# Performance work log

Measured on AMD Instinct MI355X. Metric: run time of the kernel, lower is better.

## Reference

```python
import jax, jax.numpy as jnp
import numpy as np

N_NODES = 40000
N_EDGES = 640000
NODE_D = 128
EDGE_D = 64
OUT_D = 128


def setup_inputs() -> dict:
    key = jax.random.key(0)
    ks = jax.random.split(key, 8)
    return {
        "node_features": jax.random.normal(ks[0], (N_NODES, NODE_D), dtype=jnp.float32),
        "edge_features": jax.random.normal(ks[1], (N_EDGES, EDGE_D), dtype=jnp.float32),
        "src": jax.random.randint(ks[2], (N_EDGES,), 0, N_NODES, dtype=jnp.int32),
        "dst": jax.random.randint(ks[3], (N_EDGES,), 0, N_NODES, dtype=jnp.int32),
        "W_msg_w": jax.random.normal(ks[4], (OUT_D, NODE_D + EDGE_D), dtype=jnp.float32) * 0.05,
        "W_msg_b": jax.random.normal(ks[5], (OUT_D,), dtype=jnp.float32) * 0.05,
        "W_apply_w": jax.random.normal(ks[6], (OUT_D, OUT_D + NODE_D), dtype=jnp.float32) * 0.05,
        "W_apply_b": jax.random.normal(ks[7], (OUT_D,), dtype=jnp.float32) * 0.05,
    }


def reference(node_features, edge_features, src, dst, W_msg_w, W_msg_b, W_apply_w, W_apply_b):
    n_nodes = node_features.shape[0]
    # message: gather src node feats, concat edge feats, linear + relu  [E, OUT_D]
    msg_in = jnp.concatenate([node_features[src], edge_features], axis=-1)
    m = jax.nn.relu(msg_in @ W_msg_w.T + W_msg_b)
    # aggregate: sum messages into destination nodes  [N, OUT_D]
    h_neigh = jax.ops.segment_sum(m, dst, num_segments=n_nodes)
    # apply: concat original node feats with aggregated messages, linear + relu
    apply_in = jnp.concatenate([node_features, h_neigh], axis=-1)
    return jax.nn.relu(apply_in @ W_apply_w.T + W_apply_b)
```

## Files before the change

kernel.cpp:

```cpp
#include <hip/hip_runtime.h>
#include <stdint.h>

#define NN 40000
#define NE 640000
#define ND 128
#define ED 64
#define OD 128
#define KM 192
#define KA 256
#define NB 40

typedef __attribute__((ext_vector_type(8))) short bf16x8;
typedef __attribute__((ext_vector_type(4))) float f32x4;
typedef __attribute__((ext_vector_type(4))) unsigned short us4;

__device__ __forceinline__ unsigned short f2bf(float f) {
    union { float f; uint32_t u; } v; v.f = f;
    return (unsigned short)((v.u + 0x7fffu + ((v.u >> 16) & 1u)) >> 16);
}
__device__ __forceinline__ us4 pk4(float4 v) {
    us4 r; r.x = f2bf(v.x); r.y = f2bf(v.y); r.z = f2bf(v.z); r.w = f2bf(v.w);
    return r;
}
__device__ __forceinline__ bf16x8 pk8(float4 a, float4 b) {
    bf16x8 r;
    r[0] = (short)f2bf(a.x); r[1] = (short)f2bf(a.y);
    r[2] = (short)f2bf(a.z); r[3] = (short)f2bf(a.w);
    r[4] = (short)f2bf(b.x); r[5] = (short)f2bf(b.y);
    r[6] = (short)f2bf(b.z); r[7] = (short)f2bf(b.w);
    return r;
}
__device__ __forceinline__ float bfl(uint32_t u) {
    union { uint32_t u; float f; } v; v.u = u << 16; return v.f;
}

__global__ void hist_kernel(const int* __restrict__ dst, int* __restrict__ cnt) {
    int e = blockIdx.x * blockDim.x + threadIdx.x;
    if (e < NE) atomicAdd(&cnt[dst[e]], 1);
}

__global__ __launch_bounds__(1024) void scanA_kernel(
    const int* __restrict__ cnt, int* __restrict__ off, int* __restrict__ bsum)
{
    __shared__ int wsum[16];
    const int t = threadIdx.x, b = blockIdx.x;
    const int idx = b * 1024 + t;
    int v = (idx < NN) ? cnt[idx] : 0;
    int x = v;
    #pragma unroll
    for (int d = 1; d < 64; d <<= 1) {
        int y = __shfl_up(x, d, 64);
        if ((t & 63) >= d) x += y;
    }
    const int wid = t >> 6;
    if ((t & 63) == 63) wsum[wid] = x;
    __syncthreads();
    if (t < 16) {
        int s = wsum[t];
        #pragma unroll
        for (int d = 1; d < 16; d <<= 1) {
            int y = __shfl_up(s, d, 64);
            if (t >= d) s += y;
        }
        wsum[t] = s;
    }
    __syncthreads();
    int incl = x + (wid > 0 ? wsum[wid - 1] : 0);
    if (idx < NN) off[idx] = incl - v;
    if (t == 1023) bsum[b] = incl;
}

__global__ __launch_bounds__(64) void scanB_kernel(
    const int* __restrict__ bsum, int* __restrict__ boff, int* __restrict__ off)
{
    const int t = threadIdx.x;
    int v = (t < NB) ? bsum[t] : 0;
    int x = v;
    #pragma unroll
    for (int d = 1; d < 64; d <<= 1) {
        int y = __shfl_up(x, d, 64);
        if (t >= d) x += y;
    }
    if (t < NB) boff[t] = x - v;
    if (t == 63) off[NN] = x;
}

__global__ __launch_bounds__(1024) void scanC_kernel(
    int* __restrict__ off, const int* __restrict__ boff, int* __restrict__ cur)
{
    const int idx = blockIdx.x * 1024 + threadIdx.x;
    if (idx < NN) {
        int val = off[idx] + boff[blockIdx.x];
        off[idx] = val;
        cur[idx] = val;
    }
}

__global__ void scatter_kernel(const int* __restrict__ dst, const int* __restrict__ src,
                               int* __restrict__ cur, int* __restrict__ eid,
                               int* __restrict__ srcp, int* __restrict__ dstp) {
    int e = blockIdx.x * blockDim.x + threadIdx.x;
    if (e < NE) {
        int d = dst[e];
        int p = atomicAdd(&cur[d], 1);
        eid[p]  = e;
        srcp[p] = src[e];
        dstp[p] = d;
    }
}

#define PT 32
__global__ __launch_bounds__(256, 2) void proj_kernel(
    const float* __restrict__ node, const float* __restrict__ Wm,
    unsigned short* __restrict__ P)
{
    __shared__ unsigned short sW[OD][136];
    __shared__ unsigned short sA[PT][136];
    const int t = threadIdx.x, n0 = blockIdx.x * PT;
    {
        int el = t >> 3, sub = t & 7;
        const float* np = node + (size_t)(n0 + el) * ND + sub * 16;
        #pragma unroll
        for (int i = 0; i < 4; ++i) {
            float4 v = *(const float4*)(np + i * 4);
            *(us4*)&sA[el][sub * 16 + i * 4] = pk4(v);
        }
    }
    for (int i = t; i < OD * 128 / 4; i += 256) {
        int base = i * 4;
        int n = base / 128, k = base % 128;
        float4 wv = *(const float4*)(Wm + n * KM + k);
        *(us4*)&sW[n][k] = pk4(wv);
    }
    __syncthreads();

    const int w = t >> 6, lane = t & 63, l15 = lane & 15, lhi = lane >> 4;
    const int koff = lhi * 8;
    f32x4 acc[2][2] = {};
    #pragma unroll
    for (int ks = 0; ks < 4; ++ks) {
        bf16x8 a0 = *(const bf16x8*)&sA[l15][ks * 32 + koff];
        bf16x8 a1 = *(const bf16x8*)&sA[16 + l15][ks * 32 + koff];
        bf16x8 b0 = *(const bf16x8*)&sW[w * 32 + l15][ks * 32 + koff];
        bf16x8 b1 = *(const bf16x8*)&sW[w * 32 + 16 + l15][ks * 32 + koff];
        acc[0][0] = __builtin_amdgcn_mfma_f32_16x16x32_bf16(a0, b0, acc[0][0], 0, 0, 0);
        acc[1][0] = __builtin_amdgcn_mfma_f32_16x16x32_bf16(a1, b0, acc[1][0], 0, 0, 0);
        acc[0][1] = __builtin_amdgcn_mfma_f32_16x16x32_bf16(a0, b1, acc[0][1], 0, 0, 0);
        acc[1][1] = __builtin_amdgcn_mfma_f32_16x16x32_bf16(a1, b1, acc[1][1], 0, 0, 0);
    }
    #pragma unroll
    for (int ai = 0; ai < 2; ++ai)
        #pragma unroll
        for (int r = 0; r < 4; ++r) {
            int m = n0 + ai * 16 + 4 * lhi + r;
            #pragma unroll
            for (int bj = 0; bj < 2; ++bj) {
                int n = w * 32 + bj * 16 + l15;
                P[(size_t)m * OD + n] = f2bf(acc[ai][bj][r]);
            }
        }
}

#define QT 64
#define MROW 148

__global__ __launch_bounds__(256, 4) void msgagg_kernel(
    const float* __restrict__ edgef, const int* __restrict__ eid,
    const int* __restrict__ srcp, const int* __restrict__ dstp,
    const unsigned short* __restrict__ P,
    const float* __restrict__ Wm, const float* __restrict__ bm,
    float* __restrict__ hn)
{
    __shared__ union {
        struct {
            unsigned short E[QT][72];
            unsigned short Pp[QT][136];
        } s;
        unsigned short m[QT][MROW];
    } u;
    __shared__ int sD[QT];

    const int t = threadIdx.x, j0 = blockIdx.x * QT;
    const int w = t >> 6, lane = t & 63, l15 = lane & 15, lhi = lane >> 4;

    bf16x8 bw[2][2];
    #pragma unroll
    for (int bj = 0; bj < 2; ++bj) {
        int n = w * 32 + bj * 16 + l15;
        const float* wp = Wm + n * KM + ND;
        #pragma unroll
        for (int ks = 0; ks < 2; ++ks) {
            float4 x = *(const float4*)(wp + ks * 32 + lhi * 8);
            float4 y = *(const float4*)(wp + ks * 32 + lhi * 8 + 4);
            bw[ks][bj] = pk8(x, y);
        }
    }
    float bmv[2] = { bm[w * 32 + l15], bm[w * 32 + 16 + l15] };

    {
        int row = t >> 2, s4 = t & 3;
        int e  = eid[j0 + row];
        int sp = srcp[j0 + row];
        const float* ep = edgef + (size_t)e * ED + s4 * 16;
        #pragma unroll
        for (int i = 0; i < 4; ++i) {
            float4 v = *(const float4*)(ep + i * 4);
            *(us4*)&u.s.E[row][s4 * 16 + i * 4] = pk4(v);
        }
        const uint4* pp = (const uint4*)(P + (size_t)sp * OD) + s4 * 4;
        #pragma unroll
        for (int i = 0; i < 4; ++i) {
            *(uint4*)&u.s.Pp[row][s4 * 32 + i * 8] = pp[i];
        }
    }
    if (t < QT) sD[t] = dstp[j0 + t];
    __syncthreads();

    f32x4 acc[4][2] = {};
    #pragma unroll
    for (int ks = 0; ks < 2; ++ks) {
        bf16x8 a[4];
        #pragma unroll
        for (int ai = 0; ai < 4; ++ai)
            a[ai] = *(const bf16x8*)&u.s.E[ai * 16 + l15][ks * 32 + lhi * 8];
        #pragma unroll
        for (int ai = 0; ai < 4; ++ai) {
            acc[ai][0] = __builtin_amdgcn_mfma_f32_16x16x32_bf16(a[ai], bw[ks][0], acc[ai][0], 0, 0, 0);
            acc[ai][1] = __builtin_amdgcn_mfma_f32_16x16x32_bf16(a[ai], bw[ks][1], acc[ai][1], 0, 0, 0);
        }
    }

    #pragma unroll
    for (int ai = 0; ai < 4; ++ai)
        #pragma unroll
        for (int r = 0; r < 4; ++r) {
            int m = ai * 16 + 4 * lhi + r;
            #pragma unroll
            for (int bj = 0; bj < 2; ++bj) {
                int n = w * 32 + bj * 16 + l15;
                float v = acc[ai][bj][r] + bmv[bj] + bfl(u.s.Pp[m][n]);
                acc[ai][bj][r] = v > 0.f ? v : 0.f;
            }
        }
    __syncthreads();

    #pragma unroll
    for (int ai = 0; ai < 4; ++ai)
        #pragma unroll
        for (int r = 0; r < 4; ++r) {
            int m = ai * 16 + 4 * lhi + r;
            #pragma unroll
            for (int bj = 0; bj < 2; ++bj) {
                int n = w * 32 + bj * 16 + l15;
                u.m[m][n] = f2bf(acc[ai][bj][r]);
            }
        }
    __syncthreads();

    if (t < OD) {
        const int c = t;
        int dprev = sD[0];
        int start = 0;
        float accv = bfl(u.m[0][c]);
        #pragma unroll 4
        for (int r = 1; r < QT; ++r) {
            int d = sD[r];
            float v = bfl(u.m[r][c]);
            if (d != dprev) {
                float* dest = hn + (size_t)dprev * OD + c;
                if (start > 0) *dest = accv;
                else atomicAdd(dest, accv);
                accv = v; dprev = d; start = r;
            } else {
                accv += v;
            }
        }
        atomicAdd(hn + (size_t)dprev * OD + c, accv);
    }
}

#define MT 32
#define LK (KM + 8)
__global__ __launch_bounds__(256, 2) void msg_kernel_atomic(
    const float* __restrict__ node, const float* __restrict__ edgef,
    const int* __restrict__ src, const int* __restrict__ dst,
    const float* __restrict__ Wm, const float* __restrict__ bm,
    float* __restrict__ hn)
{
    __shared__ unsigned short sW[OD][LK];
    __shared__ unsigned short sA[MT][LK];

    const int t  = threadIdx.x;
    const int e0 = blockIdx.x * MT;

    for (int i = t; i < OD * KM / 4; i += 256) {
        int base = i * 4;
        int n = base / KM, k = base % KM;
        float4 w = *(const float4*)(Wm + n * KM + k);
        *(us4*)&sW[n][k] = pk4(w);
    }
    {
        int el = t >> 3, sub = t & 7;
        int s = src[e0 + el];
        const float* np = node + (size_t)s * ND + sub * 16;
        #pragma unroll
        for (int i = 0; i < 4; ++i) {
            float4 v = *(const float4*)(np + i * 4);
            *(us4*)&sA[el][sub * 16 + i * 4] = pk4(v);
        }
        const float* ep = edgef + (size_t)(e0 + el) * ED + sub * 8;
        #pragma unroll
        for (int i = 0; i < 2; ++i) {
            float4 v = *(const float4*)(ep + i * 4);
            *(us4*)&sA[el][ND + sub * 8 + i * 4] = pk4(v);
        }
    }
    __syncthreads();

    const int w = t >> 6, lane = t & 63, l15 = lane & 15, lhi = lane >> 4;
    const int koff = lhi * 8;
    f32x4 acc[2][2] = {};

    #pragma unroll
    for (int ks = 0; ks < 6; ++ks) {
        bf16x8 a0 = *(const bf16x8*)&sA[l15][ks * 32 + koff];
        bf16x8 a1 = *(const bf16x8*)&sA[16 + l15][ks * 32 + koff];
        bf16x8 b0 = *(const bf16x8*)&sW[w * 32 + l15][ks * 32 + koff];
        bf16x8 b1 = *(const bf16x8*)&sW[w * 32 + 16 + l15][ks * 32 + koff];
        acc[0][0] = __builtin_amdgcn_mfma_f32_16x16x32_bf16(a0, b0, acc[0][0], 0, 0, 0);
        acc[1][0] = __builtin_amdgcn_mfma_f32_16x16x32_bf16(a1, b0, acc[1][0], 0, 0, 0);
        acc[0][1] = __builtin_amdgcn_mfma_f32_16x16x32_bf16(a0, b1, acc[0][1], 0, 0, 0);
        acc[1][1] = __builtin_amdgcn_mfma_f32_16x16x32_bf16(a1, b1, acc[1][1], 0, 0, 0);
    }

    #pragma unroll
    for (int ai = 0; ai < 2; ++ai)
        #pragma unroll
        for (int r = 0; r < 4; ++r) {
            int el = ai * 16 + 4 * lhi + r;
            int d  = dst[e0 + el];
            float* hrow = hn + (size_t)d * OD;
            #pragma unroll
            for (int bj = 0; bj < 2; ++bj) {
                int n = w * 32 + bj * 16 + l15;
                float v = acc[ai][bj][r] + bm[n];
                v = v > 0.f ? v : 0.f;
                atomicAdd(hrow + n, v);
            }
        }
}

#define AT 32
#define LKA (KA + 8)
#define LKW (128 + 8)

__global__ __launch_bounds__(256, 2) void apply_kernel(
    const float* __restrict__ node, const float* __restrict__ hn,
    const float* __restrict__ Wa, const float* __restrict__ ba,
    float* __restrict__ out)
{
    __shared__ unsigned short sW[OD][LKW];
    __shared__ unsigned short sA[AT][LKA];

    const int t  = threadIdx.x;
    const int n0 = blockIdx.x * AT;

    {
        int el = t >> 3, sub = t & 7;
        const float* np = node + (size_t)(n0 + el) * ND + sub * 16;
        #pragma unroll
        for (int i = 0; i < 4; ++i) {
            float4 v = *(const float4*)(np + i * 4);
            *(us4*)&sA[el][sub * 16 + i * 4] = pk4(v);
        }
        const float* hp = hn + (size_t)(n0 + el) * OD + sub * 16;
        #pragma unroll
        for (int i = 0; i < 4; ++i) {
            float4 v = *(const float4*)(hp + i * 4);
            *(us4*)&sA[el][ND + sub * 16 + i * 4] = pk4(v);
        }
    }
    for (int i = t; i < OD * 128 / 4; i += 256) {
        int base = i * 4;
        int n = base / 128, k = base % 128;
        float4 w = *(const float4*)(Wa + n * KA + k);
        *(us4*)&sW[n][k] = pk4(w);
    }
    __syncthreads();

    const int w = t >> 6, lane = t & 63, l15 = lane & 15, lhi = lane >> 4;
    const int koff = lhi * 8;
    f32x4 acc[2][2] = {};

    #pragma unroll
    for (int ks = 0; ks < 4; ++ks) {
        bf16x8 a0 = *(const bf16x8*)&sA[l15][ks * 32 + koff];
        bf16x8 a1 = *(const bf16x8*)&sA[16 + l15][ks * 32 + koff];
        bf16x8 b0 = *(const bf16x8*)&sW[w * 32 + l15][ks * 32 + koff];
        bf16x8 b1 = *(const bf16x8*)&sW[w * 32 + 16 + l15][ks * 32 + koff];
        acc[0][0] = __builtin_amdgcn_mfma_f32_16x16x32_bf16(a0, b0, acc[0][0], 0, 0, 0);
        acc[1][0] = __builtin_amdgcn_mfma_f32_16x16x32_bf16(a1, b0, acc[1][0], 0, 0, 0);
        acc[0][1] = __builtin_amdgcn_mfma_f32_16x16x32_bf16(a0, b1, acc[0][1], 0, 0, 0);
        acc[1][1] = __builtin_amdgcn_mfma_f32_16x16x32_bf16(a1, b1, acc[1][1], 0, 0, 0);
    }
    __syncthreads();
    for (int i = t; i < OD * 128 / 4; i += 256) {
        int base = i * 4;
        int n = base / 128, k = base % 128;
        float4 w = *(const float4*)(Wa + n * KA + 128 + k);
        *(us4*)&sW[n][k] = pk4(w);
    }
    __syncthreads();
    #pragma unroll
    for (int ks = 0; ks < 4; ++ks) {
        bf16x8 a0 = *(const bf16x8*)&sA[l15][128 + ks * 32 + koff];
        bf16x8 a1 = *(const bf16x8*)&sA[16 + l15][128 + ks * 32 + koff];
        bf16x8 b0 = *(const bf16x8*)&sW[w * 32 + l15][ks * 32 + koff];
        bf16x8 b1 = *(const bf16x8*)&sW[w * 32 + 16 + l15][ks * 32 + koff];
        acc[0][0] = __builtin_amdgcn_mfma_f32_16x16x32_bf16(a0, b0, acc[0][0], 0, 0, 0);
        acc[1][0] = __builtin_amdgcn_mfma_f32_16x16x32_bf16(a1, b0, acc[1][0], 0, 0, 0);
        acc[0][1] = __builtin_amdgcn_mfma_f32_16x16x32_bf16(a0, b1, acc[0][1], 0, 0, 0);
        acc[1][1] = __builtin_amdgcn_mfma_f32_16x16x32_bf16(a1, b1, acc[1][1], 0, 0, 0);
    }

    #pragma unroll
    for (int ai = 0; ai < 2; ++ai)
        #pragma unroll
        for (int r = 0; r < 4; ++r) {
            int nd = n0 + ai * 16 + 4 * lhi + r;
            #pragma unroll
            for (int bj = 0; bj < 2; ++bj) {
                int n = w * 32 + bj * 16 + l15;
                float v = acc[ai][bj][r] + ba[n];
                out[(size_t)nd * OD + n] = v > 0.f ? v : 0.f;
            }
        }
}

extern "C" void kernel_launch(void* const* d_in, const int* in_sizes, int n_in,
                              void* d_out, int out_size, void* d_ws, size_t ws_size,
                              hipStream_t stream) {
    const float* node  = (const float*)d_in[0];
    const float* edgef = (const float*)d_in[1];
    const int*   src   = (const int*)d_in[2];
    const int*   dst   = (const int*)d_in[3];
    const float* Wm    = (const float*)d_in[4];
    const float* bm    = (const float*)d_in[5];
    const float* Wa    = (const float*)d_in[6];
    const float* ba    = (const float*)d_in[7];
    float* out = (float*)d_out;

    size_t o = 0;
    const size_t o_P    = o; o += (size_t)NN * OD * 2;
    const size_t o_hn   = o; o += (size_t)NN * OD * 4;
    const size_t o_eid  = o; o += (size_t)NE * 4;
    const size_t o_srcp = o; o += (size_t)NE * 4;
    const size_t o_dstp = o; o += (size_t)NE * 4;
    const size_t o_off  = o; o += ((size_t)(NN + 1) * 4 + 15) & ~(size_t)15;
    const size_t o_cur  = o; o += (size_t)NN * 4;
    const size_t o_bsum = o; o += 64 * 4;
    const size_t o_boff = o; o += 64 * 4;
    const size_t need   = o;

    char* ws = (char*)d_ws;

    if (ws_size >= need) {
        unsigned short* P  = (unsigned short*)(ws + o_P);
        float* hn  = (float*)(ws + o_hn);
        int* eid   = (int*)(ws + o_eid);
        int* srcp  = (int*)(ws + o_srcp);
        int* dstp  = (int*)(ws + o_dstp);
        int* off   = (int*)(ws + o_off);
        int* cur   = (int*)(ws + o_cur);
        int* bsum  = (int*)(ws + o_bsum);
        int* boff  = (int*)(ws + o_boff);

        hipMemsetAsync(cur, 0, (size_t)NN * 4, stream);
        hipMemsetAsync(hn, 0, (size_t)NN * OD * 4, stream);
        hist_kernel<<<(NE + 255) / 256, 256, 0, stream>>>(dst, cur);
        scanA_kernel<<<NB, 1024, 0, stream>>>(cur, off, bsum);
        scanB_kernel<<<1, 64, 0, stream>>>(bsum, boff, off);
        scanC_kernel<<<NB, 1024, 0, stream>>>(off, boff, cur);
        scatter_kernel<<<(NE + 255) / 256, 256, 0, stream>>>(dst, src, cur, eid, srcp, dstp);
        proj_kernel<<<NN / PT, 256, 0, stream>>>(node, Wm, P);
        msgagg_kernel<<<NE / QT, 256, 0, stream>>>(edgef, eid, srcp, dstp, P, Wm, bm, hn);
        apply_kernel<<<NN / AT, 256, 0, stream>>>(node, hn, Wa, ba, out);
    } else {
        const size_t hn_bytes = (size_t)NN * OD * 4;
        float* hn = (ws_size >= hn_bytes) ? (float*)d_ws : out;
        hipMemsetAsync(hn, 0, hn_bytes, stream);
        msg_kernel_atomic<<<NE / MT, 256, 0, stream>>>(node, edgef, src, dst, Wm, bm, hn);
        apply_kernel<<<NN / AT, 256, 0, stream>>>(node, hn, Wa, ba, out);
    }
}
```

Before: 222.4 us.

## Persistent pipelined message kernel, packed edge triples, merged scan, hardware bf16 packing

Turns the message/aggregate kernel into a persistent grid-stride loop that prefetches the next tile's edge features and projected rows into registers while the current tile computes. Edge id, source and destination are packed into one int4 array so the scatter and the gather each do a single vector access. The scan drops its middle kernel by having each block reduce the preceding block sums itself. Float-to-bf16 conversion now uses the packed HIP intrinsics, and the segmented reduction is split across two halves of 128 rows so all 256 threads take part. The prefetch costs extra registers and the persistent grid has fewer blocks, so occupancy and latency hiding could suffer.

```diff
diff --git a/kernel.cpp b/kernel.cpp
--- a/kernel.cpp
+++ b/kernel.cpp
@@ -1,4 +1,5 @@
 #include <hip/hip_runtime.h>
+#include <hip/hip_bf16.h>
 #include <stdint.h>
 
 #define NN 40000
@@ -14,24 +15,32 @@
 typedef __attribute__((ext_vector_type(4))) float f32x4;
 typedef __attribute__((ext_vector_type(4))) unsigned short us4;
 
-__device__ __forceinline__ unsigned short f2bf(float f) {
-    union { float f; uint32_t u; } v; v.f = f;
-    return (unsigned short)((v.u + 0x7fffu + ((v.u >> 16) & 1u)) >> 16);
+__device__ __forceinline__ uint32_t pkbf2(float a, float b) {
+    __hip_bfloat162 h = __float22bfloat162_rn(make_float2(a, b));
+    union { __hip_bfloat162 h; uint32_t u; } cv; cv.h = h; return cv.u;
+}
+__device__ __forceinline__ unsigned short f2bf1(float f) {
+    __hip_bfloat16 h = __float2bfloat16(f);
+    union { __hip_bfloat16 h; unsigned short u; } cv; cv.h = h; return cv.u;
 }
 __device__ __forceinline__ us4 pk4(float4 v) {
-    us4 r; r.x = f2bf(v.x); r.y = f2bf(v.y); r.z = f2bf(v.z); r.w = f2bf(v.w);
-    return r;
+    union { uint2 u; us4 s; } cv;
+    cv.u.x = pkbf2(v.x, v.y);
+    cv.u.y = pkbf2(v.z, v.w);
+    return cv.s;
 }
 __device__ __forceinline__ bf16x8 pk8(float4 a, float4 b) {
-    bf16x8 r;
-    r[0] = (short)f2bf(a.x); r[1] = (short)f2bf(a.y);
-    r[2] = (short)f2bf(a.z); r[3] = (short)f2bf(a.w);
-    r[4] = (short)f2bf(b.x); r[5] = (short)f2bf(b.y);
-    r[6] = (short)f2bf(b.z); r[7] = (short)f2bf(b.w);
-    return r;
-}
-__device__ __forceinline__ float bfl(uint32_t u) {
-    union { uint32_t u; float f; } v; v.u = u << 16; return v.f;
+    union { uint4 u; bf16x8 s; } cv;
+    cv.u.x = pkbf2(a.x, a.y); cv.u.y = pkbf2(a.z, a.w);
+    cv.u.z = pkbf2(b.x, b.y); cv.u.w = pkbf2(b.z, b.w);
+    return cv.s;
+}
+__device__ __forceinline__ void st_bf4(unsigned short* p, float4 v) {
+    uint2 r; r.x = pkbf2(v.x, v.y); r.y = pkbf2(v.z, v.w);
+    *(uint2*)p = r;
+}
+__device__ __forceinline__ float b2f(unsigned short u) {
+    union { uint32_t u; float f; } v; v.u = ((uint32_t)u) << 16; return v.f;
 }
 
 __global__ void hist_kernel(const int* __restrict__ dst, int* __restrict__ cnt) {
@@ -40,12 +49,12 @@
 }
 
 __global__ __launch_bounds__(1024) void scanA_kernel(
-    const int* __restrict__ cnt, int* __restrict__ off, int* __restrict__ bsum)
+    int* __restrict__ cur, int* __restrict__ bsum)
 {
     __shared__ int wsum[16];
     const int t = threadIdx.x, b = blockIdx.x;
     const int idx = b * 1024 + t;
-    int v = (idx < NN) ? cnt[idx] : 0;
+    int v = (idx < NN) ? cur[idx] : 0;
     int x = v;
     #pragma unroll
     for (int d = 1; d < 64; d <<= 1) {
@@ -66,46 +75,34 @@
     }
     __syncthreads();
     int incl = x + (wid > 0 ? wsum[wid - 1] : 0);
-    if (idx < NN) off[idx] = incl - v;
+    if (idx < NN) cur[idx] = incl - v;
     if (t == 1023) bsum[b] = incl;
 }
 
-__global__ __launch_bounds__(64) void scanB_kernel(
-    const int* __restrict__ bsum, int* __restrict__ boff, int* __restrict__ off)
+__global__ __launch_bounds__(1024) void scanC_kernel(
+    int* __restrict__ cur, const int* __restrict__ bsum)
 {
-    const int t = threadIdx.x;
-    int v = (t < NB) ? bsum[t] : 0;
-    int x = v;
-    #pragma unroll
-    for (int d = 1; d < 64; d <<= 1) {
-        int y = __shfl_up(x, d, 64);
-        if (t >= d) x += y;
-    }
-    if (t < NB) boff[t] = x - v;
-    if (t == 63) off[NN] = x;
-}
-
-__global__ __launch_bounds__(1024) void scanC_kernel(
-    int* __restrict__ off, const int* __restrict__ boff, int* __restrict__ cur)
-{
-    const int idx = blockIdx.x * 1024 + threadIdx.x;
-    if (idx < NN) {
-        int val = off[idx] + boff[blockIdx.x];
-        off[idx] = val;
-        cur[idx] = val;
-    }
+    __shared__ int sboff;
+    const int t = threadIdx.x, b = blockIdx.x;
+    if (t < 64) {
+        int v = (t < b) ? bsum[t] : 0;
+        #pragma unroll
+        for (int d = 32; d > 0; d >>= 1) v += __shfl_down(v, d, 64);
+        if (t == 0) sboff = v;
+    }
+    __syncthreads();
+    const int idx = b * 1024 + t;
+    if (idx < NN) cur[idx] += sboff;
 }
 
 __global__ void scatter_kernel(const int* __restrict__ dst, const int* __restrict__ src,
-                               int* __restrict__ cur, int* __restrict__ eid,
-                               int* __restrict__ srcp, int* __restrict__ dstp) {
+                               int* __restrict__ cur, int4* __restrict__ tri) {
     int e = blockIdx.x * blockDim.x + threadIdx.x;
     if (e < NE) {
+        int s = src[e];
         int d = dst[e];
         int p = atomicAdd(&cur[d], 1);
-        eid[p]  = e;
-        srcp[p] = src[e];
-        dstp[p] = d;
+        tri[p] = make_int4(e, s, d, 0);
     }
 }
 
@@ -156,17 +153,17 @@
             #pragma unroll
             for (int bj = 0; bj < 2; ++bj) {
                 int n = w * 32 + bj * 16 + l15;
-                P[(size_t)m * OD + n] = f2bf(acc[ai][bj][r]);
+                P[(size_t)m * OD + n] = f2bf1(acc[ai][bj][r]);
             }
         }
 }
 
 #define QT 64
 #define MROW 148
+#define GRID_MSG 2048
 
 __global__ __launch_bounds__(256, 4) void msgagg_kernel(
-    const float* __restrict__ edgef, const int* __restrict__ eid,
-    const int* __restrict__ srcp, const int* __restrict__ dstp,
+    const float* __restrict__ edgef, const int4* __restrict__ tri,
     const unsigned short* __restrict__ P,
     const float* __restrict__ Wm, const float* __restrict__ bm,
     float* __restrict__ hn)
@@ -180,8 +177,9 @@
     } u;
     __shared__ int sD[QT];
 
-    const int t = threadIdx.x, j0 = blockIdx.x * QT;
+    const int t = threadIdx.x;
     const int w = t >> 6, lane = t & 63, l15 = lane & 15, lhi = lane >> 4;
+    const int row = t >> 2, s4 = t & 3;
 
     bf16x8 bw[2][2];
     #pragma unroll
@@ -197,86 +195,124 @@
     }
     float bmv[2] = { bm[w * 32 + l15], bm[w * 32 + 16 + l15] };
 
+    const int NT = NE / QT;
+    int tile = blockIdx.x;
+    if (tile >= NT) return;
+
+    float4 rE0, rE1, rE2, rE3;
+    uint4  rP0, rP1, rP2, rP3;
+    int4 id, idn;
+
+#define GATHER() do { \
+        const float* ep_ = edgef + (size_t)id.x * ED + s4 * 16; \
+        rE0 = *(const float4*)(ep_ + 0); \
+        rE1 = *(const float4*)(ep_ + 4); \
+        rE2 = *(const float4*)(ep_ + 8); \
+        rE3 = *(const float4*)(ep_ + 12); \
+        const uint4* pp_ = (const uint4*)(P + (size_t)id.y * OD) + s4 * 4; \
+        rP0 = pp_[0]; rP1 = pp_[1]; rP2 = pp_[2]; rP3 = pp_[3]; \
+    } while (0)
+
+    id = tri[(size_t)tile * QT + row];
+    GATHER();
     {
-        int row = t >> 2, s4 = t & 3;
-        int e  = eid[j0 + row];
-        int sp = srcp[j0 + row];
-        const float* ep = edgef + (size_t)e * ED + s4 * 16;
-        #pragma unroll
-        for (int i = 0; i < 4; ++i) {
-            float4 v = *(const float4*)(ep + i * 4);
-            *(us4*)&u.s.E[row][s4 * 16 + i * 4] = pk4(v);
-        }
-        const uint4* pp = (const uint4*)(P + (size_t)sp * OD) + s4 * 4;
-        #pragma unroll
-        for (int i = 0; i < 4; ++i) {
-            *(uint4*)&u.s.Pp[row][s4 * 32 + i * 8] = pp[i];
-        }
-    }
-    if (t < QT) sD[t] = dstp[j0 + t];
-    __syncthreads();
-
-    f32x4 acc[4][2] = {};
-    #pragma unroll
-    for (int ks = 0; ks < 2; ++ks) {
-        bf16x8 a[4];
+        int nx = tile + GRID_MSG;
+        idn = tri[(size_t)(nx < NT ? nx : 0) * QT + row];
+    }
+
+    for (;;) {
+        st_bf4(&u.s.E[row][s4 * 16 +  0], rE0);
+        st_bf4(&u.s.E[row][s4 * 16 +  4], rE1);
+        st_bf4(&u.s.E[row][s4 * 16 +  8], rE2);
+        st_bf4(&u.s.E[row][s4 * 16 + 12], rE3);
+        *(uint4*)&u.s.Pp[row][s4 * 32 +  0] = rP0;
+        *(uint4*)&u.s.Pp[row][s4 * 32 +  8] = rP1;
+        *(uint4*)&u.s.Pp[row][s4 * 32 + 16] = rP2;
+        *(uint4*)&u.s.Pp[row][s4 * 32 + 24] = rP3;
+        if (s4 == 0) sD[row] = id.z;
+        __syncthreads();
+
+        const int next = tile + GRID_MSG;
+        const bool more = next < NT;
+        if (more) {
+            id = idn;
+            GATHER();
+            int nx2 = next + GRID_MSG;
+            idn = tri[(size_t)(nx2 < NT ? nx2 : 0) * QT + row];
+        }
+
+        f32x4 acc[4][2] = {};
+        #pragma unroll
+        for (int ks = 0; ks < 2; ++ks) {
+            bf16x8 a[4];
+            #pragma unroll
+            for (int ai = 0; ai < 4; ++ai)
+                a[ai] = *(const bf16x8*)&u.s.E[ai * 16 + l15][ks * 32 + lhi * 8];
+            #pragma unroll
+            for (int ai = 0; ai < 4; ++ai) {
+                acc[ai][0] = __builtin_amdgcn_mfma_f32_16x16x32_bf16(a[ai], bw[ks][0], acc[ai][0], 0, 0, 0);
+                acc[ai][1] = __builtin_amdgcn_mfma_f32_16x16x32_bf16(a[ai], bw[ks][1], acc[ai][1], 0, 0, 0);
+            }
+        }
+
         #pragma unroll
         for (int ai = 0; ai < 4; ++ai)
-            a[ai] = *(const bf16x8*)&u.s.E[ai * 16 + l15][ks * 32 + lhi * 8];
-        #pragma unroll
-        for (int ai = 0; ai < 4; ++ai) {
-            acc[ai][0] = __builtin_amdgcn_mfma_f32_16x16x32_bf16(a[ai], bw[ks][0], acc[ai][0], 0, 0, 0);
-            acc[ai][1] = __builtin_amdgcn_mfma_f32_16x16x32_bf16(a[ai], bw[ks][1], acc[ai][1], 0, 0, 0);
-        }
-    }
-
-    #pragma unroll
-    for (int ai = 0; ai < 4; ++ai)
-        #pragma unroll
-        for (int r = 0; r < 4; ++r) {
-            int m = ai * 16 + 4 * lhi + r;
-            #pragma unroll
-            for (int bj = 0; bj < 2; ++bj) {
-                int n = w * 32 + bj * 16 + l15;
-                float v = acc[ai][bj][r] + bmv[bj] + bfl(u.s.Pp[m][n]);
-                acc[ai][bj][r] = v > 0.f ? v : 0.f;
-            }
-        }
-    __syncthreads();
-
-    #pragma unroll
-    for (int ai = 0; ai < 4; ++ai)
-        #pragma unroll
-        for (int r = 0; r < 4; ++r) {
-            int m = ai * 16 + 4 * lhi + r;
-            #pragma unroll
-            for (int bj = 0; bj < 2; ++bj) {
-                int n = w * 32 + bj * 16 + l15;
-                u.m[m][n] = f2bf(acc[ai][bj][r]);
-            }
-        }
-    __syncthreads();
-
-    if (t < OD) {
-        const int c = t;
-        int dprev = sD[0];
-        int start = 0;
-        float accv = bfl(u.m[0][c]);
-        #pragma unroll 4
-        for (int r = 1; r < QT; ++r) {
-            int d = sD[r];
-            float v = bfl(u.m[r][c]);
-            if (d != dprev) {
-                float* dest = hn + (size_t)dprev * OD + c;
-                if (start > 0) *dest = accv;
-                else atomicAdd(dest, accv);
-                accv = v; dprev = d; start = r;
-            } else {
-                accv += v;
-            }
-        }
-        atomicAdd(hn + (size_t)dprev * OD + c, accv);
-    }
+            #pragma unroll
+            for (int r = 0; r < 4; ++r) {
+                int m = ai * 16 + 4 * lhi + r;
+                #pragma unroll
+                for (int bj = 0; bj < 2; ++bj) {
+                    int n = w * 32 + bj * 16 + l15;
+                    float v = acc[ai][bj][r] + bmv[bj] + b2f(u.s.Pp[m][n]);
+                    acc[ai][bj][r] = v > 0.f ? v : 0.f;
+                }
+            }
+        __syncthreads();
+
+        #pragma unroll
+        for (int ai = 0; ai < 4; ++ai)
+            #pragma unroll
+            for (int r = 0; r < 4; ++r) {
+                int m = ai * 16 + 4 * lhi + r;
+                #pragma unroll
+                for (int bj = 0; bj < 2; ++bj) {
+                    int n = w * 32 + bj * 16 + l15;
+                    u.m[m][n] = f2bf1(acc[ai][bj][r]);
+                }
+            }
+        __syncthreads();
+
+        {
+            const int half = t >> 7;
+            const int c = t & 127;
+            const int r0 = half * 32;
+            int dprev = sD[r0];
+            int start = r0;
+            float accv = b2f(u.m[r0][c]);
+            #pragma unroll 8
+            for (int r = r0 + 1; r < r0 + 32; ++r) {
+                int d = sD[r];
+                float v = b2f(u.m[r][c]);
+                if (d != dprev) {
+                    float* dest = hn + (size_t)dprev * OD + c;
+                    if (start > r0) *dest = accv;
+                    else atomicAdd(dest, accv);
+                    accv = v; dprev = d; start = r;
+                } else {
+                    accv += v;
+                }
+            }
+            float* dest = hn + (size_t)dprev * OD + c;
+            bool cont = (half == 0) ? (sD[32] == dprev) : true;
+            if (!cont && start > r0) *dest = accv;
+            else atomicAdd(dest, accv);
+        }
+
+        if (!more) break;
+        tile = next;
+        __syncthreads();
+    }
+#undef GATHER
 }
 
 #define MT 32
@@ -453,37 +489,28 @@
     size_t o = 0;
     const size_t o_P    = o; o += (size_t)NN * OD * 2;
     const size_t o_hn   = o; o += (size_t)NN * OD * 4;
-    const size_t o_eid  = o; o += (size_t)NE * 4;
-    const size_t o_srcp = o; o += (size_t)NE * 4;
-    const size_t o_dstp = o; o += (size_t)NE * 4;
-    const size_t o_off  = o; o += ((size_t)(NN + 1) * 4 + 15) & ~(size_t)15;
+    const size_t o_tri  = o; o += (size_t)NE * 16;
     const size_t o_cur  = o; o += (size_t)NN * 4;
     const size_t o_bsum = o; o += 64 * 4;
-    const size_t o_boff = o; o += 64 * 4;
     const size_t need   = o;
 
     char* ws = (char*)d_ws;
 
     if (ws_size >= need) {
         unsigned short* P  = (unsigned short*)(ws + o_P);
-        float* hn  = (float*)(ws + o_hn);
-        int* eid   = (int*)(ws + o_eid);
-        int* srcp  = (int*)(ws + o_srcp);
-        int* dstp  = (int*)(ws + o_dstp);
-        int* off   = (int*)(ws + o_off);
-        int* cur   = (int*)(ws + o_cur);
-        int* bsum  = (int*)(ws + o_bsum);
-        int* boff  = (int*)(ws + o_boff);
+        float* hn   = (float*)(ws + o_hn);
+        int4*  tri  = (int4*)(ws + o_tri);
+        int*   cur  = (int*)(ws + o_cur);
+        int*   bsum = (int*)(ws + o_bsum);
 
         hipMemsetAsync(cur, 0, (size_t)NN * 4, stream);
         hipMemsetAsync(hn, 0, (size_t)NN * OD * 4, stream);
         hist_kernel<<<(NE + 255) / 256, 256, 0, stream>>>(dst, cur);
-        scanA_kernel<<<NB, 1024, 0, stream>>>(cur, off, bsum);
-        scanB_kernel<<<1, 64, 0, stream>>>(bsum, boff, off);
-        scanC_kernel<<<NB, 1024, 0, stream>>>(off, boff, cur);
-        scatter_kernel<<<(NE + 255) / 256, 256, 0, stream>>>(dst, src, cur, eid, srcp, dstp);
+        scanA_kernel<<<NB, 1024, 0, stream>>>(cur, bsum);
+        scanC_kernel<<<NB, 1024, 0, stream>>>(cur, bsum);
+        scatter_kernel<<<(NE + 255) / 256, 256, 0, stream>>>(dst, src, cur, tri);
         proj_kernel<<<NN / PT, 256, 0, stream>>>(node, Wm, P);
-        msgagg_kernel<<<NE / QT, 256, 0, stream>>>(edgef, eid, srcp, dstp, P, Wm, bm, hn);
+        msgagg_kernel<<<GRID_MSG, 256, 0, stream>>>(edgef, tri, P, Wm, bm, hn);
         apply_kernel<<<NN / AT, 256, 0, stream>>>(node, hn, Wa, ba, out);
     } else {
         const size_t hn_bytes = (size_t)NN * OD * 4;
```

New measurement: 213.9 us. 3.9% less time.
